# Kernel tuning notes

Measured on AMD Instinct MI355X. Metric: run time of the kernel, lower is better.

Reference implementation:

```python
import jax, jax.numpy as jnp
import numpy as np

EPS = 0.05    # geomloss: blur**p with p=1, blur=0.05
NITER = 30    # fixed Sinkhorn iterations (geomloss uses eps-scaling; fixed-eps loop is the reference math)


def _cost(x, y):
    # x:(N,3), y:(M,3) -> (N,M) Euclidean distance (p=1 ground cost)
    d2 = jnp.sum((x[:, None, :] - y[None, :, :]) ** 2, axis=-1)
    return jnp.sqrt(d2 + 1e-12)


def _sinkhorn_ot(x, y):
    # Entropic OT cost between uniform measures on x (N pts) and y (M pts), log-domain Sinkhorn.
    n, m = x.shape[0], y.shape[0]
    C = _cost(x, y)                                  # (N,M)
    log_a = jnp.full((n,), -jnp.log(jnp.float32(n)), dtype=x.dtype)
    log_b = jnp.full((m,), -jnp.log(jnp.float32(m)), dtype=x.dtype)

    def step(carry, _):
        f, g = carry
        # f_i = -eps * LSE_j( log_b_j + (g_j - C_ij)/eps )
        f = -EPS * jax.nn.logsumexp(log_b[None, :] + (g[None, :] - C) / EPS, axis=1)
        g = -EPS * jax.nn.logsumexp(log_a[:, None] + (f[:, None] - C) / EPS, axis=0)
        return (f, g), None

    f0 = jnp.zeros((n,), dtype=x.dtype)
    g0 = jnp.zeros((m,), dtype=x.dtype)
    (f, g), _ = jax.lax.scan(step, (f0, g0), None, length=NITER)
    a = jnp.exp(log_a)
    b = jnp.exp(log_b)
    return jnp.sum(a * f) + jnp.sum(b * g)


def _sinkhorn_divergence(x, y):
    # Debiased Sinkhorn divergence: S(x,y) = OT(x,y) - 0.5*OT(x,x) - 0.5*OT(y,y)
    return _sinkhorn_ot(x, y) - 0.5 * _sinkhorn_ot(x, x) - 0.5 * _sinkhorn_ot(y, y)


def setup_inputs() -> dict:
    key = jax.random.key(0)
    k1, k2 = jax.random.split(key)
    B, N, M = 8, 2048, 2048
    xyz1 = jax.random.normal(k1, (B, N, 3), dtype=jnp.float32)
    xyz2 = jax.random.normal(k2, (B, M, 3), dtype=jnp.float32)
    return {"xyz1": xyz1, "xyz2": xyz2}


def reference(xyz1, xyz2):
    # Per-batch Sinkhorn divergence, averaged over batch (original loops over b; vmap is the
    # vectorized equivalent since clouds are independent).
    losses = jax.vmap(_sinkhorn_divergence)(xyz1, xyz2)   # (B,)
    return jnp.sum(losses) / xyz1.shape[0]
```

## Files before the change

### kernel.cpp

```cpp
#include <hip/hip_runtime.h>
#include <hip/hip_cooperative_groups.h>

namespace cg = cooperative_groups;

#define NPTS    2048
#define NBATCH  8
#define NPROB   24
#define NITER   30
#define TPB     512
#define WPB     8
#define BPP     32
#define NCHUNK  32
#define COLS_PW 256

constexpr float KSC = 28.853900817779268f;
constexpr float C1f = 0.38123094930796995f;
constexpr float C2f = 0.03465735902799726f;

__device__ __forceinline__ float fexp2(float x) { return __builtin_amdgcn_exp2f(x); }
__device__ __forceinline__ float flog2(float x) { return __builtin_amdgcn_logf(x); }
__device__ __forceinline__ float fsqrt(float x) { return __builtin_amdgcn_sqrtf(x); }

__device__ __forceinline__ void problem_barrier(unsigned* arrive, unsigned* epoch,
                                                unsigned phase, int nbpp, int tid)
{
    __syncthreads();
    if (tid == 0) {
        unsigned old = __hip_atomic_fetch_add(arrive, 1u, __ATOMIC_ACQ_REL,
                                              __HIP_MEMORY_SCOPE_AGENT);
        if (old == (unsigned)(nbpp - 1)) {
            __hip_atomic_store(arrive, 0u, __ATOMIC_RELAXED, __HIP_MEMORY_SCOPE_AGENT);
            __hip_atomic_store(epoch, phase, __ATOMIC_RELEASE, __HIP_MEMORY_SCOPE_AGENT);
        } else {
            while (__hip_atomic_load(epoch, __ATOMIC_RELAXED,
                                     __HIP_MEMORY_SCOPE_AGENT) < phase) {
                __builtin_amdgcn_s_sleep(2);
            }
            __threadfence();
        }
    }
    __syncthreads();
}

__global__ __launch_bounds__(TPB, 8)
void sinkhorn_all(const float* __restrict__ xyz1,
                  const float* __restrict__ xyz2,
                  float* __restrict__ fg,
                  unsigned* __restrict__ bars,
                  float* __restrict__ out,
                  int nbpp)
{
    __shared__ float4 shC[NPTS];
    __shared__ float  shS[WPB][64];
    __shared__ double red[WPB];

    cg::grid_group grid = cg::this_grid();

    const int tid  = threadIdx.x;
    const int lane = tid & 63;
    const int warp = tid >> 6;
    const int p    = blockIdx.x % NPROB;
    const int lb   = blockIdx.x / NPROB;
    const int b    = p / 3;
    const int k    = p - 3 * b;

    const float* xb = xyz1 + (size_t)b * NPTS * 3;
    const float* yb = xyz2 + (size_t)b * NPTS * 3;
    float* fv = fg + (size_t)p * NPTS;
    float* gv = fg + (size_t)(NPROB + p) * NPTS;
    unsigned* arrive = bars + (size_t)p * 64;
    unsigned* epoch  = bars + (size_t)p * 64 + 32;

    const float* Uf = (k == 2) ? yb : xb;
    const float* Ug = (k == 0) ? yb : ((k == 1) ? xb : yb);

    auto stage_full = [&](const float* __restrict__ V, const float* __restrict__ phi) {
        const float4* V4 = (const float4*)V;
        const float4 a  = V4[3 * tid + 0];
        const float4 bb = V4[3 * tid + 1];
        const float4 cc = V4[3 * tid + 2];
        const float4 ph = *(const float4*)(phi + 4 * tid);
        const int c = 4 * tid;
        shC[c + 0] = make_float4(a.x,  a.y,  a.z,  KSC * ph.x);
        shC[c + 1] = make_float4(a.w,  bb.x, bb.y, KSC * ph.y);
        shC[c + 2] = make_float4(bb.z, bb.w, cc.x, KSC * ph.z);
        shC[c + 3] = make_float4(cc.y, cc.z, cc.w, KSC * ph.w);
    };
    auto stage_w = [&](const float* __restrict__ phi) {
        float4 ph = *(const float4*)(phi + 4 * tid);
        shC[4 * tid + 0].w = KSC * ph.x;
        shC[4 * tid + 1].w = KSC * ph.y;
        shC[4 * tid + 2].w = KSC * ph.z;
        shC[4 * tid + 3].w = KSC * ph.w;
    };

    auto do_pass = [&](const float* __restrict__ U, float* __restrict__ o) {
        __syncthreads();
        const int cbeg = warp * COLS_PW;
        for (int rb = lb; rb < NCHUNK; rb += nbpp) {
            const int row = (rb << 6) + lane;
            const float ux = U[3 * row + 0];
            const float uy = U[3 * row + 1];
            const float uz = U[3 * row + 2];
            float s0 = 0.f, s1 = 0.f, s2 = 0.f, s3 = 0.f;

            auto term = [&](const float4 v) {
                float dx = ux - v.x, dy = uy - v.y, dz = uz - v.z;
                float d2 = fmaf(dx, dx, fmaf(dy, dy, fmaf(dz, dz, 1e-12f)));
                return fexp2(fmaf(-KSC, fsqrt(d2), v.w));
            };

            #pragma unroll 2
            for (int c = cbeg; c < cbeg + COLS_PW; c += 8) {
                const float4 v0 = shC[c + 0];
                const float4 v1 = shC[c + 1];
                const float4 v2 = shC[c + 2];
                const float4 v3 = shC[c + 3];
                const float4 v4 = shC[c + 4];
                const float4 v5 = shC[c + 5];
                const float4 v6 = shC[c + 6];
                const float4 v7 = shC[c + 7];
                s0 += term(v0);
                s1 += term(v1);
                s2 += term(v2);
                s3 += term(v3);
                s0 += term(v4);
                s1 += term(v5);
                s2 += term(v6);
                s3 += term(v7);
            }
            shS[warp][lane] = (s0 + s1) + (s2 + s3);
            __syncthreads();
            if (warp == 0) {
                float t = shS[0][lane];
                #pragma unroll
                for (int w = 1; w < WPB; ++w) t += shS[w][lane];
                o[(rb << 6) + lane] = C1f - C2f * flog2(t);
            }
            __syncthreads();
        }
    };

    if (k != 0) {
        stage_full((k == 1) ? xb : yb, gv);
        __syncthreads();
    }

    for (int it = 0; it < NITER; ++it) {
        if (k == 0) stage_full(yb, gv); else stage_w(gv);
        do_pass(Uf, fv);
        problem_barrier(arrive, epoch, (unsigned)(2 * it + 1), nbpp, tid);
        if (k == 0) stage_full(xb, fv); else stage_w(fv);
        do_pass(Ug, gv);
        problem_barrier(arrive, epoch, (unsigned)(2 * it + 2), nbpp, tid);
    }

    grid.sync();

    if (blockIdx.x == 0) {
        double acc = 0.0;
        for (int idx = tid; idx < 2 * NPROB * NPTS; idx += TPB) {
            int rem = (idx < NPROB * NPTS) ? idx : idx - NPROB * NPTS;
            int pp  = rem >> 11;
            int kk  = pp % 3;
            float w = (kk == 0) ? 1.0f : -0.5f;
            acc += (double)fg[idx] * (double)w;
        }
        #pragma unroll
        for (int off = 32; off > 0; off >>= 1) acc += __shfl_xor(acc, off);
        if (lane == 0) red[warp] = acc;
        __syncthreads();
        if (warp == 0) {
            double v2 = (lane < WPB) ? red[lane] : 0.0;
            #pragma unroll
            for (int off = 32; off > 0; off >>= 1) v2 += __shfl_xor(v2, off);
            if (lane == 0) out[0] = (float)(v2 / (double)(NBATCH * NPTS));
        }
    }
}

extern "C" void kernel_launch(void* const* d_in, const int* in_sizes, int n_in,
                              void* d_out, int out_size, void* d_ws, size_t ws_size,
                              hipStream_t stream)
{
    const float* xyz1 = (const float*)d_in[0];
    const float* xyz2 = (const float*)d_in[1];
    float* out = (float*)d_out;
    float* fg  = (float*)d_ws;
    unsigned* bars = (unsigned*)((char*)d_ws + (size_t)2 * NPROB * NPTS * sizeof(float));

    hipMemsetAsync(d_ws, 0,
                   (size_t)2 * NPROB * NPTS * sizeof(float) +
                   (size_t)NPROB * 64 * sizeof(unsigned),
                   stream);

    int maxB = 0;
    hipOccupancyMaxActiveBlocksPerMultiprocessor(&maxB, sinkhorn_all, TPB, 0);
    if (maxB < 1) maxB = 1;
    int bpp = (maxB * 256) / NPROB;
    if (bpp > BPP) bpp = BPP;
    if (bpp < 1) bpp = 1;
    int nblk = NPROB * bpp;

    void* args[] = { (void*)&xyz1, (void*)&xyz2, (void*)&fg, (void*)&bars,
                     (void*)&out, (void*)&bpp };
    hipLaunchCooperativeKernel((void*)sinkhorn_all, dim3(nblk), dim3(TPB),
                               args, 0, stream);
}
```

Measured before the change: 2.652 ms.

## Split column range into halves and compute two rows per thread

Each block now handles a job made of a half of the columns (1024) and a 128-row chunk, with every thread computing two rows so that each LDS float4 read is reused twice. Partial sums for the two halves are written to global memory, and the log and the potential are rebuilt during staging of the next pass, instead of storing the potentials directly. The grid.sync is replaced by a separate final reduction kernel, and launch bounds drop to 6 blocks per CU. This adds restaging of coordinates every job and a split-sum layout, which costs extra global traffic.

```diff
diff --git a/kernel.cpp b/kernel.cpp
--- a/kernel.cpp
+++ b/kernel.cpp
@@ -1,7 +1,4 @@
 #include <hip/hip_runtime.h>
-#include <hip/hip_cooperative_groups.h>
-
-namespace cg = cooperative_groups;
 
 #define NPTS    2048
 #define NBATCH  8
@@ -9,9 +6,9 @@
 #define NITER   30
 #define TPB     512
 #define WPB     8
-#define BPP     32
-#define NCHUNK  32
-#define COLS_PW 256
+#define NJOBS   32
+#define HCOLS   1024
+#define CPW     128
 
 constexpr float KSC = 28.853900817779268f;
 constexpr float C1f = 0.38123094930796995f;
@@ -20,6 +17,13 @@
 __device__ __forceinline__ float fexp2(float x) { return __builtin_amdgcn_exp2f(x); }
 __device__ __forceinline__ float flog2(float x) { return __builtin_amdgcn_logf(x); }
 __device__ __forceinline__ float fsqrt(float x) { return __builtin_amdgcn_sqrtf(x); }
+
+__global__ __launch_bounds__(256)
+void init_sums(float* __restrict__ gsum)
+{
+    int i = blockIdx.x * 256 + threadIdx.x;
+    if (i < NPROB * 2 * NPTS) gsum[i] = 1024.0f;
+}
 
 __device__ __forceinline__ void problem_barrier(unsigned* arrive, unsigned* epoch,
                                                 unsigned phase, int nbpp, int tid)
@@ -42,19 +46,16 @@
     __syncthreads();
 }
 
-__global__ __launch_bounds__(TPB, 8)
+__global__ __launch_bounds__(TPB, 6)
 void sinkhorn_all(const float* __restrict__ xyz1,
                   const float* __restrict__ xyz2,
-                  float* __restrict__ fg,
+                  float* __restrict__ fsum,
+                  float* __restrict__ gsum,
                   unsigned* __restrict__ bars,
-                  float* __restrict__ out,
                   int nbpp)
 {
-    __shared__ float4 shC[NPTS];
-    __shared__ float  shS[WPB][64];
-    __shared__ double red[WPB];
-
-    cg::grid_group grid = cg::this_grid();
+    __shared__ float4 shC[HCOLS];
+    __shared__ float  shS[WPB][128];
 
     const int tid  = threadIdx.x;
     const int lane = tid & 63;
@@ -66,116 +67,115 @@
 
     const float* xb = xyz1 + (size_t)b * NPTS * 3;
     const float* yb = xyz2 + (size_t)b * NPTS * 3;
-    float* fv = fg + (size_t)p * NPTS;
-    float* gv = fg + (size_t)(NPROB + p) * NPTS;
+    float* fS = fsum + (size_t)p * 2 * NPTS;
+    float* gS = gsum + (size_t)p * 2 * NPTS;
     unsigned* arrive = bars + (size_t)p * 64;
     unsigned* epoch  = bars + (size_t)p * 64 + 32;
 
     const float* Uf = (k == 2) ? yb : xb;
     const float* Ug = (k == 0) ? yb : ((k == 1) ? xb : yb);
-
-    auto stage_full = [&](const float* __restrict__ V, const float* __restrict__ phi) {
-        const float4* V4 = (const float4*)V;
-        const float4 a  = V4[3 * tid + 0];
-        const float4 bb = V4[3 * tid + 1];
-        const float4 cc = V4[3 * tid + 2];
-        const float4 ph = *(const float4*)(phi + 4 * tid);
-        const int c = 4 * tid;
-        shC[c + 0] = make_float4(a.x,  a.y,  a.z,  KSC * ph.x);
-        shC[c + 1] = make_float4(a.w,  bb.x, bb.y, KSC * ph.y);
-        shC[c + 2] = make_float4(bb.z, bb.w, cc.x, KSC * ph.z);
-        shC[c + 3] = make_float4(cc.y, cc.z, cc.w, KSC * ph.w);
+    const float* Vf = (k == 1) ? xb : yb;
+    const float* Vg = (k == 2) ? yb : xb;
+
+    auto stage = [&](const float* __restrict__ V, const float* __restrict__ S, int h) {
+        if (tid < 256) {
+            const float4* V4 = (const float4*)V;
+            const int i0 = 3 * (h * 256 + tid);
+            const float4 a  = V4[i0 + 0];
+            const float4 bb = V4[i0 + 1];
+            const float4 cc = V4[i0 + 2];
+            const int c  = 4 * tid;
+            const int gc = h * HCOLS + c;
+            const float4 t0 = *(const float4*)(S + gc);
+            const float4 t1 = *(const float4*)(S + NPTS + gc);
+            shC[c + 0] = make_float4(a.x,  a.y,  a.z,  11.0f - flog2(t0.x + t1.x));
+            shC[c + 1] = make_float4(a.w,  bb.x, bb.y, 11.0f - flog2(t0.y + t1.y));
+            shC[c + 2] = make_float4(bb.z, bb.w, cc.x, 11.0f - flog2(t0.z + t1.z));
+            shC[c + 3] = make_float4(cc.y, cc.z, cc.w, 11.0f - flog2(t0.w + t1.w));
+        }
     };
-    auto stage_w = [&](const float* __restrict__ phi) {
-        float4 ph = *(const float4*)(phi + 4 * tid);
-        shC[4 * tid + 0].w = KSC * ph.x;
-        shC[4 * tid + 1].w = KSC * ph.y;
-        shC[4 * tid + 2].w = KSC * ph.z;
-        shC[4 * tid + 3].w = KSC * ph.w;
+
+    auto do_pass = [&](const float* __restrict__ U, float* __restrict__ oS,
+                       int h, int rc) {
+        __syncthreads();
+        const int r0 = rc * 128 + lane, r1 = r0 + 64;
+        const float ux0 = U[3*r0], uy0 = U[3*r0+1], uz0 = U[3*r0+2];
+        const float ux1 = U[3*r1], uy1 = U[3*r1+1], uz1 = U[3*r1+2];
+        float s00 = 0.f, s01 = 0.f, s02 = 0.f, s03 = 0.f;
+        float s10 = 0.f, s11 = 0.f, s12 = 0.f, s13 = 0.f;
+        auto term = [&](const float4 v, float ux, float uy, float uz) {
+            float dx = ux - v.x, dy = uy - v.y, dz = uz - v.z;
+            float d2 = fmaf(dx, dx, fmaf(dy, dy, fmaf(dz, dz, 1e-12f)));
+            return fexp2(fmaf(-KSC, fsqrt(d2), v.w));
+        };
+        const int cb = warp * CPW;
+        #pragma unroll 2
+        for (int c = cb; c < cb + CPW; c += 4) {
+            const float4 v0 = shC[c + 0];
+            const float4 v1 = shC[c + 1];
+            const float4 v2 = shC[c + 2];
+            const float4 v3 = shC[c + 3];
+            s00 += term(v0, ux0, uy0, uz0);  s10 += term(v0, ux1, uy1, uz1);
+            s01 += term(v1, ux0, uy0, uz0);  s11 += term(v1, ux1, uy1, uz1);
+            s02 += term(v2, ux0, uy0, uz0);  s12 += term(v2, ux1, uy1, uz1);
+            s03 += term(v3, ux0, uy0, uz0);  s13 += term(v3, ux1, uy1, uz1);
+        }
+        shS[warp][lane]      = (s00 + s01) + (s02 + s03);
+        shS[warp][lane + 64] = (s10 + s11) + (s12 + s13);
+        __syncthreads();
+        if (tid < 128) {
+            float t = shS[0][tid];
+            #pragma unroll
+            for (int w = 1; w < WPB; ++w) t += shS[w][tid];
+            oS[h * NPTS + rc * 128 + tid] = t;
+        }
+        __syncthreads();
     };
 
-    auto do_pass = [&](const float* __restrict__ U, float* __restrict__ o) {
-        __syncthreads();
-        const int cbeg = warp * COLS_PW;
-        for (int rb = lb; rb < NCHUNK; rb += nbpp) {
-            const int row = (rb << 6) + lane;
-            const float ux = U[3 * row + 0];
-            const float uy = U[3 * row + 1];
-            const float uz = U[3 * row + 2];
-            float s0 = 0.f, s1 = 0.f, s2 = 0.f, s3 = 0.f;
-
-            auto term = [&](const float4 v) {
-                float dx = ux - v.x, dy = uy - v.y, dz = uz - v.z;
-                float d2 = fmaf(dx, dx, fmaf(dy, dy, fmaf(dz, dz, 1e-12f)));
-                return fexp2(fmaf(-KSC, fsqrt(d2), v.w));
-            };
-
-            #pragma unroll 2
-            for (int c = cbeg; c < cbeg + COLS_PW; c += 8) {
-                const float4 v0 = shC[c + 0];
-                const float4 v1 = shC[c + 1];
-                const float4 v2 = shC[c + 2];
-                const float4 v3 = shC[c + 3];
-                const float4 v4 = shC[c + 4];
-                const float4 v5 = shC[c + 5];
-                const float4 v6 = shC[c + 6];
-                const float4 v7 = shC[c + 7];
-                s0 += term(v0);
-                s1 += term(v1);
-                s2 += term(v2);
-                s3 += term(v3);
-                s0 += term(v4);
-                s1 += term(v5);
-                s2 += term(v6);
-                s3 += term(v7);
-            }
-            shS[warp][lane] = (s0 + s1) + (s2 + s3);
-            __syncthreads();
-            if (warp == 0) {
-                float t = shS[0][lane];
-                #pragma unroll
-                for (int w = 1; w < WPB; ++w) t += shS[w][lane];
-                o[(rb << 6) + lane] = C1f - C2f * flog2(t);
-            }
-            __syncthreads();
-        }
-    };
-
-    if (k != 0) {
-        stage_full((k == 1) ? xb : yb, gv);
-        __syncthreads();
-    }
-
     for (int it = 0; it < NITER; ++it) {
-        if (k == 0) stage_full(yb, gv); else stage_w(gv);
-        do_pass(Uf, fv);
+        for (int j = lb; j < NJOBS; j += nbpp) {
+            stage(Vf, gS, j & 1);
+            do_pass(Uf, fS, j & 1, j >> 1);
+        }
         problem_barrier(arrive, epoch, (unsigned)(2 * it + 1), nbpp, tid);
-        if (k == 0) stage_full(xb, fv); else stage_w(fv);
-        do_pass(Ug, gv);
+        for (int j = lb; j < NJOBS; j += nbpp) {
+            stage(Vg, fS, j & 1);
+            do_pass(Ug, gS, j & 1, j >> 1);
+        }
         problem_barrier(arrive, epoch, (unsigned)(2 * it + 2), nbpp, tid);
     }
-
-    grid.sync();
-
-    if (blockIdx.x == 0) {
-        double acc = 0.0;
-        for (int idx = tid; idx < 2 * NPROB * NPTS; idx += TPB) {
-            int rem = (idx < NPROB * NPTS) ? idx : idx - NPROB * NPTS;
-            int pp  = rem >> 11;
-            int kk  = pp % 3;
-            float w = (kk == 0) ? 1.0f : -0.5f;
-            acc += (double)fg[idx] * (double)w;
-        }
+}
+
+__global__ __launch_bounds__(TPB, 1)
+void final_reduce(const float* __restrict__ fsum, const float* __restrict__ gsum,
+                  float* __restrict__ out)
+{
+    __shared__ double red[WPB];
+    const int tid  = threadIdx.x;
+    const int lane = tid & 63;
+    const int warp = tid >> 6;
+
+    double acc = 0.0;
+    for (int idx = tid; idx < 2 * NPROB * NPTS; idx += TPB) {
+        const bool isF = idx < NPROB * NPTS;
+        const int rem  = isF ? idx : idx - NPROB * NPTS;
+        const int pp   = rem >> 11;
+        const int j    = rem & (NPTS - 1);
+        const float* S = (isF ? fsum : gsum) + (size_t)pp * 2 * NPTS;
+        const float t  = S[j] + S[NPTS + j];
+        const float val = C1f - C2f * flog2(t);
+        const float w   = (pp % 3 == 0) ? 1.0f : -0.5f;
+        acc += (double)val * (double)w;
+    }
+    #pragma unroll
+    for (int off = 32; off > 0; off >>= 1) acc += __shfl_xor(acc, off);
+    if (lane == 0) red[warp] = acc;
+    __syncthreads();
+    if (warp == 0) {
+        double v2 = (lane < WPB) ? red[lane] : 0.0;
         #pragma unroll
-        for (int off = 32; off > 0; off >>= 1) acc += __shfl_xor(acc, off);
-        if (lane == 0) red[warp] = acc;
-        __syncthreads();
-        if (warp == 0) {
-            double v2 = (lane < WPB) ? red[lane] : 0.0;
-            #pragma unroll
-            for (int off = 32; off > 0; off >>= 1) v2 += __shfl_xor(v2, off);
-            if (lane == 0) out[0] = (float)(v2 / (double)(NBATCH * NPTS));
-        }
+        for (int off = 32; off > 0; off >>= 1) v2 += __shfl_xor(v2, off);
+        if (lane == 0) out[0] = (float)(v2 / (double)(NBATCH * NPTS));
     }
 }
 
@@ -186,24 +186,26 @@
     const float* xyz1 = (const float*)d_in[0];
     const float* xyz2 = (const float*)d_in[1];
     float* out = (float*)d_out;
-    float* fg  = (float*)d_ws;
-    unsigned* bars = (unsigned*)((char*)d_ws + (size_t)2 * NPROB * NPTS * sizeof(float));
-
-    hipMemsetAsync(d_ws, 0,
-                   (size_t)2 * NPROB * NPTS * sizeof(float) +
-                   (size_t)NPROB * 64 * sizeof(unsigned),
-                   stream);
+
+    float* fsum = (float*)d_ws;
+    float* gsum = fsum + (size_t)NPROB * 2 * NPTS;
+    unsigned* bars = (unsigned*)(gsum + (size_t)NPROB * 2 * NPTS);
+
+    hipMemsetAsync(bars, 0, (size_t)NPROB * 64 * sizeof(unsigned), stream);
+    init_sums<<<(NPROB * 2 * NPTS + 255) / 256, 256, 0, stream>>>(gsum);
 
     int maxB = 0;
     hipOccupancyMaxActiveBlocksPerMultiprocessor(&maxB, sinkhorn_all, TPB, 0);
     if (maxB < 1) maxB = 1;
     int bpp = (maxB * 256) / NPROB;
-    if (bpp > BPP) bpp = BPP;
+    if (bpp > NJOBS) bpp = NJOBS;
     if (bpp < 1) bpp = 1;
     int nblk = NPROB * bpp;
 
-    void* args[] = { (void*)&xyz1, (void*)&xyz2, (void*)&fg, (void*)&bars,
-                     (void*)&out, (void*)&bpp };
+    void* args[] = { (void*)&xyz1, (void*)&xyz2, (void*)&fsum, (void*)&gsum,
+                     (void*)&bars, (void*)&bpp };
     hipLaunchCooperativeKernel((void*)sinkhorn_all, dim3(nblk), dim3(TPB),
                                args, 0, stream);
-}
+
+    final_reduce<<<1, TPB, 0, stream>>>(fsum, gsum, out);
+}
```

After: 2.655 ms. No clear change (+0.1%).
